# Kernel optimization log

Measured on AMD Instinct MI355X. Metric: run time of the kernel, lower is better.

Reference implementation:

```python
import jax, jax.numpy as jnp
import numpy as np

BATCH, SEQ, DIN, FILTERS, KSIZE = 64, 512, 256, 256, 3

def setup_inputs() -> dict:
    key = jax.random.key(0)
    ks = jax.random.split(key, 5)
    s_u = 1.0 / np.sqrt(DIN)
    return {
        "x": jax.random.normal(ks[0], (BATCH, SEQ, DIN), dtype=jnp.float32),
        "z": jax.random.normal(ks[1], (BATCH, DIN), dtype=jnp.float32),
        "U": jax.random.normal(ks[2], (DIN, DIN), dtype=jnp.float32) * s_u,
        "V": jax.random.normal(ks[3], (DIN, KSIZE * FILTERS), dtype=jnp.float32) * s_u,
        "B_w": jax.random.normal(ks[4], (DIN, KSIZE * FILTERS), dtype=jnp.float32) * s_u,
        "b": jnp.zeros((FILTERS,), dtype=jnp.float32),
        "kernel_size": KSIZE,
    }

def reference(x, z, U, V, B_w, b, kernel_size):
    Bn, L, din = x.shape
    K = int(kernel_size)
    F = V.shape[1] // K
    # per-sample dynamic kernel: (U * sigmoid(z)) @ V + B
    zf = jax.nn.sigmoid(z)                                  # (B, din)
    f = jnp.einsum('de,be,ef->bdf', U, zf, V) + B_w[None]    # (B, din, K*F)
    f = f.reshape(Bn, din, K, F).transpose(0, 2, 1, 3)       # (B, K, din, F)
    # 'same' padding, stride 1
    pad_l, pad_r = (K - 1) // 2, K // 2
    xp = jnp.pad(x, ((0, 0), (pad_l, pad_r), (0, 0)))        # (B, L+K-1, din)
    patches = jnp.stack([xp[:, i:i + L] for i in range(K)], axis=2)  # (B, L, K, din)
    out = jnp.einsum('blkd,bkdf->blf', patches, f) + b       # (B, L, F)
    return jax.nn.relu(out)
```

## Files before the change

kernel.cpp:

```cpp
#include <hip/hip_runtime.h>
#include <math.h>

#define BATCH 64
#define SEQL  512
#define DIN   256
#define NF    256
#define KS    3
#define KF    (KS * NF)

#define XCH 512
#define KC  (KS * XCH)
#define PR2 66
#define PLD 128
#define P0SZ (PR2 * PLD)

typedef __attribute__((ext_vector_type(8))) short short8;
typedef __attribute__((ext_vector_type(4))) float floatx4;
typedef __attribute__((ext_vector_type(16))) float floatx16;
typedef __attribute__((ext_vector_type(8))) unsigned short ushort8v;
typedef __attribute__((ext_vector_type(4))) unsigned short ushort4v;

static __device__ __forceinline__ unsigned short f2bf(float f) {
    unsigned int u = __float_as_uint(f);
    return (unsigned short)((u + 0x7FFF + ((u >> 16) & 1)) >> 16);
}

__global__ __launch_bounds__(256) void pack_kernel(
    const float* __restrict__ U, const float* __restrict__ V,
    const float* __restrict__ Bw,
    unsigned short* __restrict__ WcTp, unsigned short* __restrict__ UTp)
{
    const int blk = blockIdx.x;
    const int t   = threadIdx.x;

    if (blk < 96) {
        const int gk = blk >> 3;
        const int g  = gk / 3, k = gk % 3;
        const int ks = t >> 5;
        const int f  = (blk & 7) * 32 + (t & 31);
        unsigned short* dst = WcTp + ((size_t)(gk * 8 + ks) * 256 + f) * 16;
        #pragma unroll
        for (int c = 0; c < 16; ++c) {
            const int ch = g * 128 + ks * 16 + c;
            const float v = (ch < DIN)
                ? Bw[(size_t)ch * KF + k * NF + f]
                : V[(size_t)(ch - DIN) * KF + k * NF + f];
            dst[c] = f2bf(v);
        }
    } else {
        const int bb = blk - 96;
        const int kk = bb >> 1;
        const int e0 = (bb & 1) * 128;
        #pragma unroll
        for (int it = 0; it < 2; ++it) {
            const int p    = t + it * 256;
            const int e    = e0 + (p >> 2);
            const int quad = p & 3;
            unsigned short* dst =
                UTp + ((size_t)(kk * 256 + e) * 4 + quad) * 8;
            #pragma unroll
            for (int c = 0; c < 8; ++c) {
                const int d = kk * 32 + quad * 8 + c;
                dst[c] = f2bf(U[(size_t)d * DIN + e]);
            }
        }
    }
}

__global__ __launch_bounds__(256, 2) void fused_kernel(
    const float* __restrict__ x, const float* __restrict__ z,
    const unsigned short* __restrict__ UTp,
    const unsigned short* __restrict__ WcTp,
    const float* __restrict__ bias, float* __restrict__ out)
{
    __shared__ __align__(16) unsigned short lds[4 * P0SZ];

    const int tid  = threadIdx.x;
    const int lane = tid & 63;
    const int wave = tid >> 6;
    const int quad = lane >> 4, l16 = lane & 15;
    const int l32  = lane & 31, hi  = lane >> 5;

    const int bid = blockIdx.x;
    const int b   = bid >> 3;
    const int l0  = (bid & 7) * 64;

    #pragma unroll
    for (int p = 0; p < 2; ++p) {
        unsigned short* P = lds + (size_t)p * P0SZ;
        #pragma unroll
        for (int it = 0; it < 5; ++it) {
            const int idx = tid + it * 256;
            if (idx < PR2 * 16) {
                const int row = idx >> 4, u = idx & 15;
                const int l = l0 - 1 + row;
                ushort8v h = {};
                if (l >= 0 && l < SEQL) {
                    const float* xp =
                        x + ((size_t)b * SEQL + l) * DIN + p * 128 + u * 8;
                    const float4 v0 = *(const float4*)xp;
                    const float4 v1 = *(const float4*)(xp + 4);
                    h[0] = f2bf(v0.x); h[1] = f2bf(v0.y);
                    h[2] = f2bf(v0.z); h[3] = f2bf(v0.w);
                    h[4] = f2bf(v1.x); h[5] = f2bf(v1.y);
                    h[6] = f2bf(v1.z); h[7] = f2bf(v1.w);
                }
                *(ushort8v*)&P[row * PLD + ((u ^ (row & 15)) << 3)] = h;
            }
        }
    }
    __syncthreads();

    {
        floatx4 accY[4][5] = {};
        #pragma unroll 2
        for (int kk = 0; kk < 8; ++kk) {
            const unsigned short* P = lds + (size_t)(kk >> 2) * P0SZ;
            const int ux = (kk & 3) * 4 + quad;
            short8 uf[4];
            #pragma unroll
            for (int q = 0; q < 4; ++q) {
                const int e = q * 64 + wave * 16 + l16;
                uf[q] = *(const short8*)
                    &UTp[((size_t)(kk * 256 + e) * 4 + quad) * 8];
            }
            #pragma unroll
            for (int i = 0; i < 5; ++i) {
                const int row = i * 16 + l16;
                const short8 xf = *(const short8*)
                    &P[row * PLD + ((ux ^ (row & 15)) << 3)];
                #pragma unroll
                for (int q = 0; q < 4; ++q)
                    accY[q][i] = __builtin_amdgcn_mfma_f32_16x16x32_bf16(
                        uf[q], xf, accY[q][i], 0, 0, 0);
            }
        }
        #pragma unroll
        for (int q = 0; q < 4; ++q) {
            const int e0 = q * 64 + wave * 16 + quad * 4;
            unsigned short* PY = lds + (size_t)(2 + (q >> 1)) * P0SZ;
            const int c0 = e0 & 127;
            float zf[4];
            #pragma unroll
            for (int r2 = 0; r2 < 4; ++r2)
                zf[r2] = 1.0f / (1.0f + expf(-z[(size_t)b * DIN + e0 + r2]));
            const int u = c0 >> 3;
            #pragma unroll
            for (int i = 0; i < 5; ++i) {
                const int xrow = i * 16 + l16;
                if (xrow < PR2) {
                    ushort4v h;
                    #pragma unroll
                    for (int r2 = 0; r2 < 4; ++r2)
                        h[r2] = f2bf(accY[q][i][r2] * zf[r2]);
                    *(ushort4v*)&PY[xrow * PLD + ((u ^ (xrow & 15)) << 3) +
                                    (c0 & 7)] = h;
                }
            }
        }
    }
    __syncthreads();

    floatx16 acc2[2][2] = {};
    #pragma unroll 1
    for (int gg = 0; gg < 4; ++gg) {
        const int g = (gg + (bid & 3)) & 3;
        const unsigned short* P = lds + (size_t)g * P0SZ;
        #pragma unroll
        for (int k = 0; k < KS; ++k) {
            const unsigned short* gW =
                WcTp + (size_t)(g * 3 + k) * 8 * 4096;
            #pragma unroll
            for (int ks = 0; ks < 8; ++ks) {
                short8 af[2], bf[2];
                const int ua = ks * 2 + hi;
                #pragma unroll
                for (int i = 0; i < 2; ++i) {
                    const int m = i * 32 + l32 + k;
                    af[i] = *(const short8*)
                        &P[m * PLD + ((ua ^ (m & 15)) << 3)];
                }
                #pragma unroll
                for (int j = 0; j < 2; ++j) {
                    const int f = wave * 64 + j * 32 + l32;
                    bf[j] = *(const short8*)
                        &gW[(size_t)ks * 4096 + (size_t)f * 16 + hi * 8];
                }
                #pragma unroll
                for (int i = 0; i < 2; ++i)
                    #pragma unroll
                    for (int j = 0; j < 2; ++j)
                        acc2[i][j] = __builtin_amdgcn_mfma_f32_32x32x16_bf16(
                            af[i], bf[j], acc2[i][j], 0, 0, 0);
            }
        }
    }

    #pragma unroll
    for (int j = 0; j < 2; ++j) {
        const int f  = wave * 64 + j * 32 + l32;
        const float bv = bias[f];
        #pragma unroll
        for (int i = 0; i < 2; ++i) {
            #pragma unroll
            for (int reg = 0; reg < 16; ++reg) {
                const int rowl = i * 32 + (reg & 3) + 8 * (reg >> 2) + 4 * hi;
                const float v = acc2[i][j][reg] + bv;
                out[((size_t)b * SEQL + l0 + rowl) * NF + f] = fmaxf(v, 0.0f);
            }
        }
    }
}

extern "C" void kernel_launch(void* const* d_in, const int* in_sizes, int n_in,
                              void* d_out, int out_size, void* d_ws, size_t ws_size,
                              hipStream_t stream) {
    const float* x    = (const float*)d_in[0];
    const float* z    = (const float*)d_in[1];
    const float* U    = (const float*)d_in[2];
    const float* V    = (const float*)d_in[3];
    const float* Bw   = (const float*)d_in[4];
    const float* bias = (const float*)d_in[5];

    unsigned short* WcTp = (unsigned short*)d_ws;
    unsigned short* UTp  = WcTp + (size_t)12 * 8 * 256 * 16;
    float* out = (float*)d_out;

    pack_kernel<<<dim3(112), 256, 0, stream>>>(U, V, Bw, WcTp, UTp);
    fused_kernel<<<dim3(512), 256, 0, stream>>>(x, z, UTp, WcTp, bias, out);
}
```

Measured before the change: 124.6 us.

## Double-buffer global weight loads in registers and raise MFMA wave priority

Both GEMM phases now prefetch the next step's global operands (U fragments and packed conv weights) into a second register buffer before running the current step's MFMAs. The intent is to hide global-memory latency behind matrix math. The first weight tile is loaded before the sigmoid-scaling epilogue of the first phase. The MFMA sections are also wrapped in s_setprio. The cost is many more live VGPRs (two 16-entry short8 buffers plus the accumulators) under launch_bounds(256,2), which risks spills or lower occupancy.

Result: faster. 121.7 us (-2.3%).

```diff
diff --git a/kernel.cpp b/kernel.cpp
--- a/kernel.cpp
+++ b/kernel.cpp
@@ -84,6 +84,18 @@
     const int bid = blockIdx.x;
     const int b   = bid >> 3;
     const int l0  = (bid & 7) * 64;
+
+    short8 uA[4], uB[4];
+    auto loadU = [&](int kk, short8 (&buf)[4]) {
+        #pragma unroll
+        for (int q = 0; q < 4; ++q) {
+            const int e = q * 64 + wave * 16 + l16;
+            buf[q] = *(const short8*)
+                &UTp[((size_t)(kk * 256 + e) * 4 + quad) * 8];
+        }
+    };
+
+    loadU(0, uA);
 
     #pragma unroll
     for (int p = 0; p < 2; ++p) {
@@ -111,19 +123,12 @@
     }
     __syncthreads();
 
+    floatx4 accY[4][5] = {};
     {
-        floatx4 accY[4][5] = {};
-        #pragma unroll 2
-        for (int kk = 0; kk < 8; ++kk) {
+        auto computeG = [&](int kk, const short8 (&buf)[4]) {
             const unsigned short* P = lds + (size_t)(kk >> 2) * P0SZ;
             const int ux = (kk & 3) * 4 + quad;
-            short8 uf[4];
-            #pragma unroll
-            for (int q = 0; q < 4; ++q) {
-                const int e = q * 64 + wave * 16 + l16;
-                uf[q] = *(const short8*)
-                    &UTp[((size_t)(kk * 256 + e) * 4 + quad) * 8];
-            }
+            __builtin_amdgcn_s_setprio(1);
             #pragma unroll
             for (int i = 0; i < 5; ++i) {
                 const int row = i * 16 + l16;
@@ -132,47 +137,72 @@
                 #pragma unroll
                 for (int q = 0; q < 4; ++q)
                     accY[q][i] = __builtin_amdgcn_mfma_f32_16x16x32_bf16(
-                        uf[q], xf, accY[q][i], 0, 0, 0);
-            }
-        }
-        #pragma unroll
-        for (int q = 0; q < 4; ++q) {
-            const int e0 = q * 64 + wave * 16 + quad * 4;
-            unsigned short* PY = lds + (size_t)(2 + (q >> 1)) * P0SZ;
-            const int c0 = e0 & 127;
-            float zf[4];
-            #pragma unroll
-            for (int r2 = 0; r2 < 4; ++r2)
-                zf[r2] = 1.0f / (1.0f + expf(-z[(size_t)b * DIN + e0 + r2]));
-            const int u = c0 >> 3;
-            #pragma unroll
-            for (int i = 0; i < 5; ++i) {
-                const int xrow = i * 16 + l16;
-                if (xrow < PR2) {
-                    ushort4v h;
-                    #pragma unroll
-                    for (int r2 = 0; r2 < 4; ++r2)
-                        h[r2] = f2bf(accY[q][i][r2] * zf[r2]);
-                    *(ushort4v*)&PY[xrow * PLD + ((u ^ (xrow & 15)) << 3) +
-                                    (c0 & 7)] = h;
-                }
+                        buf[q], xf, accY[q][i], 0, 0, 0);
+            }
+            __builtin_amdgcn_s_setprio(0);
+        };
+        #pragma unroll 1
+        for (int kb = 0; kb < 4; ++kb) {
+            const int kk = kb * 2;
+            loadU(kk + 1, uB);
+            computeG(kk, uA);
+            if (kk + 2 < 8) loadU(kk + 2, uA);
+            computeG(kk + 1, uB);
+        }
+    }
+
+    short8 bA[16], bB[16];
+    auto loadB = [&](int r, short8 (&buf)[16]) {
+        const int gg = r / 3, k = r - gg * 3;
+        const int g  = (gg + (bid & 3)) & 3;
+        const unsigned short* gW = WcTp + (size_t)(g * 3 + k) * 8 * 4096;
+        #pragma unroll
+        for (int ks = 0; ks < 8; ++ks)
+            #pragma unroll
+            for (int j = 0; j < 2; ++j) {
+                const int f = wave * 64 + j * 32 + l32;
+                buf[ks * 2 + j] = *(const short8*)
+                    &gW[(size_t)ks * 4096 + (size_t)f * 16 + hi * 8];
+            }
+    };
+
+    loadB(0, bA);
+
+    #pragma unroll
+    for (int q = 0; q < 4; ++q) {
+        const int e0 = q * 64 + wave * 16 + quad * 4;
+        unsigned short* PY = lds + (size_t)(2 + (q >> 1)) * P0SZ;
+        const int c0 = e0 & 127;
+        float zf[4];
+        #pragma unroll
+        for (int r2 = 0; r2 < 4; ++r2)
+            zf[r2] = 1.0f / (1.0f + expf(-z[(size_t)b * DIN + e0 + r2]));
+        const int u = c0 >> 3;
+        #pragma unroll
+        for (int i = 0; i < 5; ++i) {
+            const int xrow = i * 16 + l16;
+            if (xrow < PR2) {
+                ushort4v h;
+                #pragma unroll
+                for (int r2 = 0; r2 < 4; ++r2)
+                    h[r2] = f2bf(accY[q][i][r2] * zf[r2]);
+                *(ushort4v*)&PY[xrow * PLD + ((u ^ (xrow & 15)) << 3) +
+                                (c0 & 7)] = h;
             }
         }
     }
     __syncthreads();
 
     floatx16 acc2[2][2] = {};
-    #pragma unroll 1
-    for (int gg = 0; gg < 4; ++gg) {
-        const int g = (gg + (bid & 3)) & 3;
-        const unsigned short* P = lds + (size_t)g * P0SZ;
-        #pragma unroll
-        for (int k = 0; k < KS; ++k) {
-            const unsigned short* gW =
-                WcTp + (size_t)(g * 3 + k) * 8 * 4096;
+    {
+        auto computeB = [&](int r, const short8 (&buf)[16]) {
+            const int gg = r / 3, k = r - gg * 3;
+            const int g  = (gg + (bid & 3)) & 3;
+            const unsigned short* P = lds + (size_t)g * P0SZ;
+            __builtin_amdgcn_s_setprio(1);
             #pragma unroll
             for (int ks = 0; ks < 8; ++ks) {
-                short8 af[2], bf[2];
+                short8 af[2];
                 const int ua = ks * 2 + hi;
                 #pragma unroll
                 for (int i = 0; i < 2; ++i) {
@@ -181,18 +211,21 @@
                         &P[m * PLD + ((ua ^ (m & 15)) << 3)];
                 }
                 #pragma unroll
-                for (int j = 0; j < 2; ++j) {
-                    const int f = wave * 64 + j * 32 + l32;
-                    bf[j] = *(const short8*)
-                        &gW[(size_t)ks * 4096 + (size_t)f * 16 + hi * 8];
-                }
-                #pragma unroll
                 for (int i = 0; i < 2; ++i)
                     #pragma unroll
                     for (int j = 0; j < 2; ++j)
                         acc2[i][j] = __builtin_amdgcn_mfma_f32_32x32x16_bf16(
-                            af[i], bf[j], acc2[i][j], 0, 0, 0);
-            }
+                            af[i], buf[ks * 2 + j], acc2[i][j], 0, 0, 0);
+            }
+            __builtin_amdgcn_s_setprio(0);
+        };
+        #pragma unroll 1
+        for (int rr = 0; rr < 6; ++rr) {
+            const int r = rr * 2;
+            loadB(r + 1, bB);
+            computeB(r, bA);
+            if (r + 2 < 12) loadB(r + 2, bA);
+            computeB(r + 1, bB);
         }
     }
 
```

## Software-pipeline global weight loads with register ring buffers and MFMA priority

Applied to the files above, without the earlier changes.

U-fragment loads for the first GEMM are issued before the x staging and then prefetched three iterations ahead through a 4-slot register ring. The second GEMM's weight fragments are split into 24 half-stages with the same ring, and the first three are prefetched before the Y epilogue and barrier. s_setprio is raised around the MFMA blocks. The goal is to hide global load latency behind compute, at the cost of many more live registers (cb alone is 128 VGPRs), which may cause spills or lower occupancy under launch_bounds(256,2).

Measured after the change: 133.7 us. 7.3% more time.

```diff
diff --git a/kernel.cpp b/kernel.cpp
--- a/kernel.cpp
+++ b/kernel.cpp
@@ -84,6 +84,18 @@
     const int bid = blockIdx.x;
     const int b   = bid >> 3;
     const int l0  = (bid & 7) * 64;
+
+    short8 uf[4][4];
+    auto loadU = [&](int kk, int s) {
+        #pragma unroll
+        for (int q = 0; q < 4; ++q) {
+            const int e = q * 64 + wave * 16 + l16;
+            uf[s][q] = *(const short8*)
+                &UTp[((size_t)(kk * 256 + e) * 4 + quad) * 8];
+        }
+    };
+
+    loadU(0, 0); loadU(1, 1); loadU(2, 2);
 
     #pragma unroll
     for (int p = 0; p < 2; ++p) {
@@ -111,19 +123,15 @@
     }
     __syncthreads();
 
+    floatx4 accY[4][5] = {};
     {
-        floatx4 accY[4][5] = {};
-        #pragma unroll 2
+        #pragma unroll
         for (int kk = 0; kk < 8; ++kk) {
+            if (kk + 3 < 8) loadU(kk + 3, (kk + 3) & 3);
             const unsigned short* P = lds + (size_t)(kk >> 2) * P0SZ;
             const int ux = (kk & 3) * 4 + quad;
-            short8 uf[4];
-            #pragma unroll
-            for (int q = 0; q < 4; ++q) {
-                const int e = q * 64 + wave * 16 + l16;
-                uf[q] = *(const short8*)
-                    &UTp[((size_t)(kk * 256 + e) * 4 + quad) * 8];
-            }
+            const int s  = kk & 3;
+            __builtin_amdgcn_s_setprio(1);
             #pragma unroll
             for (int i = 0; i < 5; ++i) {
                 const int row = i * 16 + l16;
@@ -132,47 +140,72 @@
                 #pragma unroll
                 for (int q = 0; q < 4; ++q)
                     accY[q][i] = __builtin_amdgcn_mfma_f32_16x16x32_bf16(
-                        uf[q], xf, accY[q][i], 0, 0, 0);
-            }
-        }
-        #pragma unroll
-        for (int q = 0; q < 4; ++q) {
-            const int e0 = q * 64 + wave * 16 + quad * 4;
-            unsigned short* PY = lds + (size_t)(2 + (q >> 1)) * P0SZ;
-            const int c0 = e0 & 127;
-            float zf[4];
-            #pragma unroll
-            for (int r2 = 0; r2 < 4; ++r2)
-                zf[r2] = 1.0f / (1.0f + expf(-z[(size_t)b * DIN + e0 + r2]));
-            const int u = c0 >> 3;
-            #pragma unroll
-            for (int i = 0; i < 5; ++i) {
-                const int xrow = i * 16 + l16;
-                if (xrow < PR2) {
-                    ushort4v h;
-                    #pragma unroll
-                    for (int r2 = 0; r2 < 4; ++r2)
-                        h[r2] = f2bf(accY[q][i][r2] * zf[r2]);
-                    *(ushort4v*)&PY[xrow * PLD + ((u ^ (xrow & 15)) << 3) +
-                                    (c0 & 7)] = h;
-                }
+                        uf[s][q], xf, accY[q][i], 0, 0, 0);
+            }
+            __builtin_amdgcn_s_setprio(0);
+        }
+    }
+
+    short8 cb[4][8];
+    auto loadH = [&](int h, int s) {
+        const int r  = h >> 1;
+        const int gg = r / 3, k = r - gg * 3;
+        const int g  = (gg + (bid & 3)) & 3;
+        const unsigned short* gW = WcTp + (size_t)(g * 3 + k) * 8 * 4096;
+        const int ks0 = (h & 1) * 4;
+        #pragma unroll
+        for (int ks2 = 0; ks2 < 4; ++ks2)
+            #pragma unroll
+            for (int j = 0; j < 2; ++j) {
+                const int f = wave * 64 + j * 32 + l32;
+                cb[s][ks2 * 2 + j] = *(const short8*)
+                    &gW[(size_t)(ks0 + ks2) * 4096 + (size_t)f * 16 + hi * 8];
+            }
+    };
+
+    loadH(0, 0); loadH(1, 1); loadH(2, 2);
+
+    #pragma unroll
+    for (int q = 0; q < 4; ++q) {
+        const int e0 = q * 64 + wave * 16 + quad * 4;
+        unsigned short* PY = lds + (size_t)(2 + (q >> 1)) * P0SZ;
+        const int c0 = e0 & 127;
+        float zf[4];
+        #pragma unroll
+        for (int r2 = 0; r2 < 4; ++r2)
+            zf[r2] = 1.0f / (1.0f + expf(-z[(size_t)b * DIN + e0 + r2]));
+        const int u = c0 >> 3;
+        #pragma unroll
+        for (int i = 0; i < 5; ++i) {
+            const int xrow = i * 16 + l16;
+            if (xrow < PR2) {
+                ushort4v h;
+                #pragma unroll
+                for (int r2 = 0; r2 < 4; ++r2)
+                    h[r2] = f2bf(accY[q][i][r2] * zf[r2]);
+                *(ushort4v*)&PY[xrow * PLD + ((u ^ (xrow & 15)) << 3) +
+                                (c0 & 7)] = h;
             }
         }
     }
     __syncthreads();
 
     floatx16 acc2[2][2] = {};
-    #pragma unroll 1
-    for (int gg = 0; gg < 4; ++gg) {
-        const int g = (gg + (bid & 3)) & 3;
-        const unsigned short* P = lds + (size_t)g * P0SZ;
-        #pragma unroll
-        for (int k = 0; k < KS; ++k) {
-            const unsigned short* gW =
-                WcTp + (size_t)(g * 3 + k) * 8 * 4096;
-            #pragma unroll
-            for (int ks = 0; ks < 8; ++ks) {
-                short8 af[2], bf[2];
+    {
+        #pragma unroll
+        for (int h = 0; h < 24; ++h) {
+            if (h + 3 < 24) loadH(h + 3, (h + 3) & 3);
+            const int r  = h >> 1;
+            const int gg = r / 3, k = r - gg * 3;
+            const int g  = (gg + (bid & 3)) & 3;
+            const unsigned short* P = lds + (size_t)g * P0SZ;
+            const int ks0 = (h & 1) * 4;
+            const int s   = h & 3;
+            __builtin_amdgcn_s_setprio(1);
+            #pragma unroll
+            for (int ks2 = 0; ks2 < 4; ++ks2) {
+                const int ks = ks0 + ks2;
+                short8 af[2];
                 const int ua = ks * 2 + hi;
                 #pragma unroll
                 for (int i = 0; i < 2; ++i) {
@@ -181,18 +214,13 @@
                         &P[m * PLD + ((ua ^ (m & 15)) << 3)];
                 }
                 #pragma unroll
-                for (int j = 0; j < 2; ++j) {
-                    const int f = wave * 64 + j * 32 + l32;
-                    bf[j] = *(const short8*)
-                        &gW[(size_t)ks * 4096 + (size_t)f * 16 + hi * 8];
-                }
-                #pragma unroll
                 for (int i = 0; i < 2; ++i)
                     #pragma unroll
                     for (int j = 0; j < 2; ++j)
                         acc2[i][j] = __builtin_amdgcn_mfma_f32_32x32x16_bf16(
-                            af[i], bf[j], acc2[i][j], 0, 0, 0);
-            }
+                            af[i], cb[s][ks2 * 2 + j], acc2[i][j], 0, 0, 0);
+            }
+            __builtin_amdgcn_s_setprio(0);
         }
     }
 
```
